# Performance work log

Measured on AMD Instinct MI355X. Metric: run time of the kernel, lower is better.

## Reference

```python
import jax, jax.numpy as jnp
import numpy as np

HIDDEN = 7168
N_HEADS = 32
QK_NOPE = 128
QK_ROPE = 64
V_DIM = 128
Q_LORA = 1536
KV_LORA = 512
ROPE_THETA = 10000.0
EPS = 1e-6
T = 2048
W_SCALE = 0.02


def setup_inputs() -> dict:
    key = jax.random.key(0)
    ks = jax.random.split(key, 8)
    return {
        "hidden_states": jax.random.normal(ks[0], (T, HIDDEN), jnp.float32),
        "positions": jnp.arange(T, dtype=jnp.int32),
        "wq_a": jax.random.normal(ks[1], (HIDDEN, Q_LORA), jnp.float32) * W_SCALE,
        "q_a_ln_w": jnp.ones((Q_LORA,), jnp.float32),
        "wq_b": jax.random.normal(ks[2], (Q_LORA, N_HEADS * (QK_NOPE + QK_ROPE)), jnp.float32) * W_SCALE,
        "wkv_a": jax.random.normal(ks[3], (HIDDEN, KV_LORA + QK_ROPE), jnp.float32) * W_SCALE,
        "kv_a_ln_w": jnp.ones((KV_LORA,), jnp.float32),
        "wkv_b": jax.random.normal(ks[4], (KV_LORA, N_HEADS * (QK_NOPE + V_DIM)), jnp.float32) * W_SCALE,
        "wo": jax.random.normal(ks[5], (N_HEADS * V_DIM, HIDDEN), jnp.float32) * W_SCALE,
    }


def _rmsnorm(x, w, eps=EPS):
    var = jnp.mean(jnp.square(x), axis=-1, keepdims=True)
    return x * jax.lax.rsqrt(var + eps) * w


def _rope_cos_sin(positions):
    # deepseek rope: base**(arange(0, d, 2)/d), interleaved (non-neox) layout
    inv_freq = 1.0 / (ROPE_THETA ** (jnp.arange(0, QK_ROPE, 2, dtype=jnp.float32) / QK_ROPE))
    ang = positions.astype(jnp.float32)[:, None] * inv_freq[None, :]  # [T, 32]
    return jnp.cos(ang), jnp.sin(ang)


def _apply_rope_interleaved(x, cos, sin):
    # x: [T, H, QK_ROPE]; even/odd interleaved pairs
    x1 = x[..., 0::2]
    x2 = x[..., 1::2]
    c = cos[:, None, :]
    s = sin[:, None, :]
    o1 = x1 * c - x2 * s
    o2 = x1 * s + x2 * c
    return jnp.stack([o1, o2], axis=-1).reshape(x.shape)


def reference(hidden_states, positions, wq_a, q_a_ln_w, wq_b, wkv_a, kv_a_ln_w, wkv_b, wo):
    scaling = (QK_NOPE + QK_ROPE) ** -0.5
    # q low-rank path: a-proj -> RMSNorm -> b-proj
    q = _rmsnorm(hidden_states @ wq_a, q_a_ln_w) @ wq_b  # [T, H*192]
    q = q.reshape(T, N_HEADS, QK_NOPE + QK_ROPE)
    q_nope, q_rope = q[..., :QK_NOPE], q[..., QK_NOPE:]
    # kv low-rank path
    latent = hidden_states @ wkv_a  # [T, KV_LORA + QK_ROPE]
    c_kv, k_rope = latent[:, :KV_LORA], latent[:, KV_LORA:]
    c_kv = _rmsnorm(c_kv, kv_a_ln_w)
    # decoupled RoPE on q_rope and shared k_rope
    cos, sin = _rope_cos_sin(positions)
    q_rope = _apply_rope_interleaved(q_rope, cos, sin)
    k_rope = _apply_rope_interleaved(k_rope[:, None, :], cos, sin)  # [T,1,64]
    # expand latent to per-head k_nope and v (kv_b_proj)
    kv = (c_kv @ wkv_b).reshape(T, N_HEADS, QK_NOPE + V_DIM)
    k_nope, v = kv[..., :QK_NOPE], kv[..., QK_NOPE:]
    k = jnp.concatenate([k_nope, jnp.broadcast_to(k_rope, (T, N_HEADS, QK_ROPE))], axis=-1)
    qf = jnp.concatenate([q_nope, q_rope], axis=-1)  # [T,H,192]
    # causal MHA
    scores = jnp.einsum("qhd,khd->hqk", qf, k) * scaling
    mask = jnp.tril(jnp.ones((T, T), dtype=bool))
    scores = jnp.where(mask[None], scores, -jnp.inf)
    p = jax.nn.softmax(scores, axis=-1)
    attn = jnp.einsum("hqk,khd->qhd", p, v).reshape(T, N_HEADS * V_DIM)
    return attn @ wo  # [T, HIDDEN]
```

## Files before the change

kernel.cpp:

```cpp
#include <hip/hip_runtime.h>
#include <stdint.h>

#define T_SEQ 2048
#define HID 7168
#define NH 32
#define DN 128
#define DR 64
#define DQK 192
#define DV 128
#define QL 1536
#define KVL 512
#define LATD 576
#define QD 6144
#define KVD 8192
#define WOK 4096
#define NCAT 2112

typedef unsigned short u16;
typedef __bf16 bf16x8 __attribute__((ext_vector_type(8)));
typedef float f32x4 __attribute__((ext_vector_type(4)));

__device__ __forceinline__ u16 f2bf(float f) {
  union { float f; unsigned u; } v; v.f = f;
  unsigned r = v.u + 0x7FFFu + ((v.u >> 16) & 1u);
  return (u16)(r >> 16);
}
__device__ __forceinline__ float bf2f(u16 s) {
  union { unsigned u; float f; } v; v.u = ((unsigned)s) << 16;
  return v.f;
}

__device__ __forceinline__ void gl2lds16(const void* g, void* l) {
  __builtin_amdgcn_global_load_lds((const __attribute__((address_space(1))) void*)g,
                                   (__attribute__((address_space(3))) void*)l, 16, 0, 0);
}

__device__ __forceinline__ f32x4 mfma16(bf16x8 a, bf16x8 b, f32x4 c) {
  return __builtin_amdgcn_mfma_f32_16x16x32_bf16(a, b, c, 0, 0, 0);
}

__device__ __forceinline__ void store_out(float* p, float v) { *p = v; }
__device__ __forceinline__ void store_out(u16* p, float v) { *p = f2bf(v); }

#define FENCE() asm volatile("" ::: "memory")

__global__ __launch_bounds__(256) void k_cvt_bf16(const float* __restrict__ in,
                                                  u16* __restrict__ out, long long n) {
  long long i = ((long long)blockIdx.x * 256 + threadIdx.x) * 8;
  if (i >= n) return;
  const float4* p = (const float4*)(in + i);
  float4 a = p[0], b = p[1];
  union { uint4 v; u16 s[8]; } o;
  o.s[0]=f2bf(a.x); o.s[1]=f2bf(a.y); o.s[2]=f2bf(a.z); o.s[3]=f2bf(a.w);
  o.s[4]=f2bf(b.x); o.s[5]=f2bf(b.y); o.s[6]=f2bf(b.z); o.s[7]=f2bf(b.w);
  *(uint4*)(out + i) = o.v;
}

__global__ __launch_bounds__(256) void k_transpose_bf16(const float* __restrict__ in,
                                                        u16* __restrict__ out, int R, int C,
                                                        float scale) {
  __shared__ float tile[64][65];
  int c0 = blockIdx.x * 64, r0 = blockIdx.y * 64;
  int tx = threadIdx.x & 15, ty = threadIdx.x >> 4;
  #pragma unroll
  for (int i = 0; i < 4; i++) {
    int r = ty + i * 16;
    float4 v = *(const float4*)(in + (size_t)(r0 + r) * C + c0 + tx * 4);
    tile[r][tx*4+0] = v.x; tile[r][tx*4+1] = v.y; tile[r][tx*4+2] = v.z; tile[r][tx*4+3] = v.w;
  }
  __syncthreads();
  #pragma unroll
  for (int i = 0; i < 4; i++) {
    int oc = ty + i * 16;
    union { uint2 v; u16 s[4]; } o;
    #pragma unroll
    for (int j = 0; j < 4; j++) o.s[j] = f2bf(tile[tx*4+j][oc] * scale);
    *(uint2*)(out + (size_t)(c0 + oc) * R + r0 + tx * 4) = o.v;
  }
}

__global__ __launch_bounds__(256) void k_rmsnorm_bf16(const float* __restrict__ x,
                                                      const float* __restrict__ w,
                                                      u16* __restrict__ out, int n, int ldin) {
  int row = blockIdx.x;
  const float* xr = x + (size_t)row * ldin;
  u16* orow = out + (size_t)row * n;
  float ss = 0.f;
  for (int i = threadIdx.x * 4; i < n; i += 1024) {
    float4 v = *(const float4*)(xr + i);
    ss += v.x*v.x + v.y*v.y + v.z*v.z + v.w*v.w;
  }
  #pragma unroll
  for (int off = 32; off > 0; off >>= 1) ss += __shfl_xor(ss, off);
  __shared__ float red[4];
  if ((threadIdx.x & 63) == 0) red[threadIdx.x >> 6] = ss;
  __syncthreads();
  float tot = red[0] + red[1] + red[2] + red[3];
  float rstd = rsqrtf(tot / (float)n + 1e-6f);
  for (int i = threadIdx.x * 4; i < n; i += 1024) {
    float4 v = *(const float4*)(xr + i);
    float4 g = *(const float4*)(w + i);
    union { uint2 u; u16 s[4]; } o;
    o.s[0]=f2bf(v.x*rstd*g.x); o.s[1]=f2bf(v.y*rstd*g.y);
    o.s[2]=f2bf(v.z*rstd*g.z); o.s[3]=f2bf(v.w*rstd*g.w);
    *(uint2*)(orow + i) = o.u;
  }
}

__global__ __launch_bounds__(256) void k_gemm_bt(const u16* __restrict__ A,
                                                 const u16* __restrict__ Bt,
                                                 float* __restrict__ C,
                                                 int M, int N, int K) {
  __shared__ __attribute__((aligned(16))) u16 As[128 * 32];
  __shared__ __attribute__((aligned(16))) u16 Bs[128 * 32];
  int m0 = blockIdx.y * 128, n0 = blockIdx.x * 128;
  int tid = threadIdx.x;
  int w = tid >> 6, lane = tid & 63, l16 = lane & 15, lh = lane >> 4;
  int wr = (w >> 1) * 64, wc = (w & 1) * 64;
  f32x4 zero = {0.f, 0.f, 0.f, 0.f};
  f32x4 acc[4][4];
  #pragma unroll
  for (int i = 0; i < 4; i++)
    #pragma unroll
    for (int j = 0; j < 4; j++) acc[i][j] = zero;
  int ra = tid >> 2, ca = (tid & 3) * 8;
  const u16* a0 = A + (size_t)(m0 + ra) * K + ca;
  const u16* a1 = A + (size_t)(m0 + ra + 64) * K + ca;
  int rb0 = n0 + ra;      rb0 = rb0 < N ? rb0 : N - 1;
  int rb1 = n0 + ra + 64; rb1 = rb1 < N ? rb1 : N - 1;
  const u16* b0 = Bt + (size_t)rb0 * K + ca;
  const u16* b1 = Bt + (size_t)rb1 * K + ca;
  for (int k0 = 0; k0 < K; k0 += 32) {
    gl2lds16(a0 + k0, &As[tid * 8]);
    gl2lds16(a1 + k0, &As[2048 + tid * 8]);
    gl2lds16(b0 + k0, &Bs[tid * 8]);
    gl2lds16(b1 + k0, &Bs[2048 + tid * 8]);
    __syncthreads();
    bf16x8 af[4], bv[4];
    #pragma unroll
    for (int i = 0; i < 4; i++) af[i] = *(const bf16x8*)&As[(wr + i * 16 + l16) * 32 + lh * 8];
    #pragma unroll
    for (int j = 0; j < 4; j++) bv[j] = *(const bf16x8*)&Bs[(wc + j * 16 + l16) * 32 + lh * 8];
    #pragma unroll
    for (int i = 0; i < 4; i++)
      #pragma unroll
      for (int j = 0; j < 4; j++)
        acc[i][j] = mfma16(af[i], bv[j], acc[i][j]);
    __syncthreads();
  }
  #pragma unroll
  for (int i = 0; i < 4; i++) {
    #pragma unroll
    for (int j = 0; j < 4; j++) {
      int col = n0 + wc + j * 16 + l16;
      if (col < N) {
        #pragma unroll
        for (int r = 0; r < 4; r++) {
          int row = m0 + wr + i * 16 + lh * 4 + r;
          C[(size_t)row * N + col] = acc[i][j][r];
        }
      }
    }
  }
}

template <typename OutT>
__global__ __launch_bounds__(512) void k_gemm_bt256(const u16* __restrict__ A,
                                                    const u16* __restrict__ Bt,
                                                    OutT* __restrict__ C,
                                                    int N, int K) {
  __shared__ __attribute__((aligned(16))) u16 lds[3 * 16384];
  const int tid = threadIdx.x;
  const int lane = tid & 63, l16 = lane & 15, lh = lane >> 4;
  const int w = tid >> 6, wm = w >> 2, wn = w & 3;
  const int m0 = blockIdx.y * 256, n0 = blockIdx.x * 256;
  const int nt = K >> 5;

  f32x4 acc[8][4];
  #pragma unroll
  for (int i = 0; i < 8; i++)
    #pragma unroll
    for (int j = 0; j < 4; j++) acc[i][j] = f32x4{0.f, 0.f, 0.f, 0.f};

  const int P = tid * 16;
  const int ls = P ^ (((P >> 7) & 7) << 4);
  const int sr = ls >> 6;
  const int sce = (ls & 63) >> 1;
  const u16* gA0 = A + (size_t)(m0 + sr) * K + sce;
  const u16* gA1 = A + (size_t)(m0 + sr + 128) * K + sce;
  const u16* gB0 = Bt + (size_t)(n0 + sr) * K + sce;
  const u16* gB1 = Bt + (size_t)(n0 + sr + 128) * K + sce;
  u16* ldst = &lds[tid * 8];

  for (int pt = 0; pt < 2 && pt < nt; ++pt) {
    gl2lds16(gA0 + pt * 32, ldst + pt * 16384);
    gl2lds16(gA1 + pt * 32, ldst + pt * 16384 + 4096);
    gl2lds16(gB0 + pt * 32, ldst + pt * 16384 + 8192);
    gl2lds16(gB1 + pt * 32, ldst + pt * 16384 + 12288);
  }
  __syncthreads();

  int bufr = 0;
  for (int t = 0; t < nt; ++t) {
    const bool more = (t + 2) < nt;
    const int bw = (t + 2) % 3;
    const u16* As = &lds[bufr * 16384];
    const u16* Bs = &lds[bufr * 16384 + 8192];
    bf16x8 afr[4], bfr[4];
    #pragma unroll
    for (int j = 0; j < 4; ++j) {
      int L = ((wn * 64 + j * 16 + l16) << 6) + (lh << 4);
      bfr[j] = *(const bf16x8*)((const char*)Bs + (L ^ (((L >> 7) & 7) << 4)));
    }
    #pragma unroll
    for (int i = 0; i < 4; ++i) {
      int L = ((wm * 128 + i * 16 + l16) << 6) + (lh << 4);
      afr[i] = *(const bf16x8*)((const char*)As + (L ^ (((L >> 7) & 7) << 4)));
    }
    if (more) {
      gl2lds16(gA0 + (t + 2) * 32, ldst + bw * 16384);
      gl2lds16(gA1 + (t + 2) * 32, ldst + bw * 16384 + 4096);
    }
    FENCE();
    __builtin_amdgcn_s_barrier();
    FENCE();
    __builtin_amdgcn_s_setprio(1);
    #pragma unroll
    for (int i = 0; i < 4; ++i)
      #pragma unroll
      for (int j = 0; j < 4; ++j)
        acc[i][j] = mfma16(afr[i], bfr[j], acc[i][j]);
    __builtin_amdgcn_s_setprio(0);
    FENCE();
    __builtin_amdgcn_s_barrier();
    FENCE();
    #pragma unroll
    for (int i = 0; i < 4; ++i) {
      int L = ((wm * 128 + 64 + i * 16 + l16) << 6) + (lh << 4);
      afr[i] = *(const bf16x8*)((const char*)As + (L ^ (((L >> 7) & 7) << 4)));
    }
    if (more) {
      gl2lds16(gB0 + (t + 2) * 32, ldst + bw * 16384 + 8192);
      gl2lds16(gB1 + (t + 2) * 32, ldst + bw * 16384 + 12288);
    }
    FENCE();
    __builtin_amdgcn_s_barrier();
    FENCE();
    __builtin_amdgcn_s_setprio(1);
    #pragma unroll
    for (int i = 0; i < 4; ++i)
      #pragma unroll
      for (int j = 0; j < 4; ++j)
        acc[4 + i][j] = mfma16(afr[i], bfr[j], acc[4 + i][j]);
    __builtin_amdgcn_s_setprio(0);
    FENCE();
    if (more) asm volatile("s_waitcnt vmcnt(4)" ::: "memory");
    else      asm volatile("s_waitcnt vmcnt(0)" ::: "memory");
    __builtin_amdgcn_s_barrier();
    FENCE();
    bufr = (bufr == 2) ? 0 : bufr + 1;
  }

  #pragma unroll
  for (int hf = 0; hf < 2; ++hf) {
    #pragma unroll
    for (int i = 0; i < 4; ++i) {
      int rbase = m0 + wm * 128 + hf * 64 + i * 16 + lh * 4;
      #pragma unroll
      for (int j = 0; j < 4; ++j) {
        int col = n0 + wn * 64 + j * 16 + l16;
        #pragma unroll
        for (int r = 0; r < 4; ++r)
          store_out(&C[(size_t)(rbase + r) * N + col], acc[hf * 4 + i][j][r]);
      }
    }
  }
}

__global__ __launch_bounds__(256) void k_build_q(const u16* __restrict__ qf,
                                                 const int* __restrict__ pos,
                                                 u16* __restrict__ Qc) {
  int t = blockIdx.x;
  __shared__ float cs[32], sn[32];
  if (threadIdx.x < 32) {
    float inv = expf(-9.2103403719761836f * (float)threadIdx.x / 32.f);
    float ang = (float)pos[t] * inv;
    cs[threadIdx.x] = cosf(ang);
    sn[threadIdx.x] = sinf(ang);
  }
  __syncthreads();
  const u16* qrow = qf + (size_t)t * QD;
  for (int e = threadIdx.x; e < QD; e += 256) {
    int h = e / 192, d = e - h * 192;
    u16 outv;
    if (d < DN) {
      outv = qrow[e];
    } else {
      int dr = d - DN, i = dr >> 1;
      float x1 = bf2f(qrow[h * 192 + DN + 2 * i]), x2 = bf2f(qrow[h * 192 + DN + 2 * i + 1]);
      float v = (dr & 1) ? (x1 * sn[i] + x2 * cs[i]) : (x1 * cs[i] - x2 * sn[i]);
      outv = f2bf(v);
    }
    Qc[((size_t)h * T_SEQ + t) * DQK + d] = outv;
  }
}

__global__ __launch_bounds__(256) void k_build_k(const u16* __restrict__ kvf,
                                                 const float* __restrict__ kr, int krld,
                                                 const int* __restrict__ pos,
                                                 u16* __restrict__ Kc) {
  int t = blockIdx.x;
  __shared__ u16 kro[64];
  if (threadIdx.x < 32) {
    int i = threadIdx.x;
    float inv = expf(-9.2103403719761836f * (float)i / 32.f);
    float ang = (float)pos[t] * inv;
    float c = cosf(ang), s = sinf(ang);
    float x1 = kr[(size_t)t * krld + 2 * i];
    float x2 = kr[(size_t)t * krld + 2 * i + 1];
    kro[2 * i]     = f2bf(x1 * c - x2 * s);
    kro[2 * i + 1] = f2bf(x1 * s + x2 * c);
  }
  __syncthreads();
  const u16* krow = kvf + (size_t)t * KVD;
  for (int e = threadIdx.x; e < NH * DQK; e += 256) {
    int h = e / 192, d = e - h * 192;
    Kc[((size_t)h * T_SEQ + t) * DQK + d] = (d < DN) ? krow[h * 256 + d] : kro[d - DN];
  }
}

__global__ __launch_bounds__(256) void k_build_vt(const u16* __restrict__ kvf,
                                                  u16* __restrict__ Vt) {
  __shared__ unsigned tile[64][65];
  int t0 = blockIdx.x * 64, d0 = blockIdx.y * 64, h = blockIdx.z;
  int tid = threadIdx.x;
  #pragma unroll
  for (int i = 0; i < 2; i++) {
    int r = (tid >> 3) + i * 32;
    int c = (tid & 7) * 8;
    uint4 v = *(const uint4*)(kvf + (size_t)(t0 + r) * KVD + h * 256 + DN + d0 + c);
    const u16* s = (const u16*)&v;
    #pragma unroll
    for (int j = 0; j < 8; j++) tile[r][c + j] = s[j];
  }
  __syncthreads();
  #pragma unroll
  for (int i = 0; i < 2; i++) {
    int d = (tid >> 3) + i * 32;
    int tb = (tid & 7) * 8;
    union { uint4 v; u16 s[8]; } o;
    #pragma unroll
    for (int j = 0; j < 8; j++) o.s[j] = (u16)tile[tb + j][d];
    *(uint4*)(Vt + ((size_t)h * DV + d0 + d) * T_SEQ + t0 + tb) = o.v;
  }
}

__global__ __launch_bounds__(256, 2) void k_mla_attn(const u16* __restrict__ Qc,
                                                     const u16* __restrict__ Kc,
                                                     const u16* __restrict__ Vt,
                                                     u16* __restrict__ attn) {
  __shared__ __attribute__((aligned(16))) u16 Ks[2 * 64 * 192];
  __shared__ __attribute__((aligned(16))) u16 Ps[64 * 64];
  int bid = blockIdx.x;
  int hi = bid >> 8, r = bid & 255;
  int qt = 31 - (r >> 3);
  int h = (hi << 3) | (r & 7);
  int tid = threadIdx.x, w = tid >> 6, lane = tid & 63, l16 = lane & 15, lh = lane >> 4;
  int swz = (l16 & 7) << 4;

  const char* Kb = (const char*)(Kc + (size_t)h * T_SEQ * DQK);
  const u16* Vh = Vt + (size_t)h * DV * T_SEQ;

  const char* Qg = (const char*)(Qc + ((size_t)h * T_SEQ + (size_t)qt * 64) * DQK);
  #pragma unroll
  for (int i = 0; i < 6; i++) {
    int L = tid * 16 + i * 4096;
    int row = L / 384;
    gl2lds16(Qg + (L ^ ((row & 7) << 4)), (char*)Ks + L);
  }
  #pragma unroll
  for (int i = 0; i < 6; i++) {
    int L = tid * 16 + i * 4096;
    int row = L / 384;
    gl2lds16(Kb + (L ^ ((row & 7) << 4)), (char*)Ks + 24576 + L);
  }
  __syncthreads();
  bf16x8 aq[6];
  #pragma unroll
  for (int kf = 0; kf < 6; kf++)
    aq[kf] = *(const bf16x8*)((const char*)Ks + (w * 16 + l16) * 384 + ((kf * 64 + lh * 16) ^ swz));
  __syncthreads();

  f32x4 zero = {0.f, 0.f, 0.f, 0.f};
  f32x4 accO[8];
  #pragma unroll
  for (int i = 0; i < 8; i++) accO[i] = zero;
  float m[4]    = {-3e38f, -3e38f, -3e38f, -3e38f};
  float lsum[4] = {0.f, 0.f, 0.f, 0.f};

  for (int kt = 0; kt <= qt; ++kt) {
    const char* Kcur = (const char*)Ks + (1 - (kt & 1)) * 24576;
    char* Kstg = (char*)Ks + (kt & 1) * 24576;
    if (kt < qt) {
      const char* Kg = Kb + (size_t)(kt + 1) * 64 * DQK * 2;
      #pragma unroll
      for (int i = 0; i < 6; i++) {
        int L = tid * 16 + i * 4096;
        int row = L / 384;
        gl2lds16(Kg + (L ^ ((row & 7) << 4)), Kstg + L);
      }
    }
    bf16x8 vf[16];
    #pragma unroll
    for (int of = 0; of < 8; ++of)
      #pragma unroll
      for (int kf = 0; kf < 2; ++kf)
        vf[of * 2 + kf] = *(const bf16x8*)(Vh + (size_t)(of * 16 + l16) * T_SEQ +
                                           kt * 64 + kf * 32 + lh * 8);

    f32x4 sf[4];
    #pragma unroll
    for (int j = 0; j < 4; j++) sf[j] = zero;
    #pragma unroll
    for (int kf = 0; kf < 6; ++kf) {
      #pragma unroll
      for (int j = 0; j < 4; ++j) {
        bf16x8 bk = *(const bf16x8*)(Kcur + (j * 16 + l16) * 384 + ((kf * 64 + lh * 16) ^ swz));
        sf[j] = mfma16(aq[kf], bk, sf[j]);
      }
    }
    bool diag = (kt == qt);
    #pragma unroll
    for (int rr = 0; rr < 4; ++rr) {
      int qrow = qt * 64 + w * 16 + lh * 4 + rr;
      float rowm = -3e38f;
      #pragma unroll
      for (int j = 0; j < 4; ++j) {
        float s = sf[j][rr];
        if (diag && (kt * 64 + j * 16 + l16) > qrow) s = -3e38f;
        sf[j][rr] = s;
        rowm = fmaxf(rowm, s);
      }
      rowm = fmaxf(rowm, __shfl_xor(rowm, 1));
      rowm = fmaxf(rowm, __shfl_xor(rowm, 2));
      rowm = fmaxf(rowm, __shfl_xor(rowm, 4));
      rowm = fmaxf(rowm, __shfl_xor(rowm, 8));
      float mnew = fmaxf(m[rr], rowm);
      float sc = __expf(m[rr] - mnew);
      float pj[4];
      float ps = 0.f;
      #pragma unroll
      for (int j = 0; j < 4; ++j) { pj[j] = __expf(sf[j][rr] - mnew); ps += pj[j]; }
      ps += __shfl_xor(ps, 1); ps += __shfl_xor(ps, 2);
      ps += __shfl_xor(ps, 4); ps += __shfl_xor(ps, 8);
      lsum[rr] = lsum[rr] * sc + ps;
      m[rr] = mnew;
      #pragma unroll
      for (int of = 0; of < 8; ++of) accO[of][rr] *= sc;
      int rw = w * 16 + lh * 4 + rr;
      int rsw = (rw & 7) << 4;
      #pragma unroll
      for (int j = 0; j < 4; ++j)
        *(u16*)((char*)Ps + rw * 128 + ((2 * (j * 16 + l16)) ^ rsw)) = f2bf(pj[j]);
    }
    #pragma unroll
    for (int kf = 0; kf < 2; ++kf) {
      bf16x8 ap = *(const bf16x8*)((const char*)Ps + (w * 16 + l16) * 128 +
                                   ((kf * 64 + lh * 16) ^ swz));
      #pragma unroll
      for (int of = 0; of < 8; ++of)
        accO[of] = mfma16(ap, vf[of * 2 + kf], accO[of]);
    }
    __syncthreads();
  }
  #pragma unroll
  for (int rr = 0; rr < 4; ++rr) {
    float inv = 1.f / lsum[rr];
    int t = qt * 64 + w * 16 + lh * 4 + rr;
    #pragma unroll
    for (int of = 0; of < 8; ++of)
      attn[(size_t)t * WOK + h * DV + of * 16 + l16] = f2bf(accO[of][rr] * inv);
  }
}

extern "C" void kernel_launch(void* const* d_in, const int* in_sizes, int n_in,
                              void* d_out, int out_size, void* d_ws, size_t ws_size,
                              hipStream_t stream) {
  const float* hidden     = (const float*)d_in[0];
  const int*   positions  = (const int*)d_in[1];
  const float* wq_a       = (const float*)d_in[2];
  const float* q_a_ln_w   = (const float*)d_in[3];
  const float* wq_b       = (const float*)d_in[4];
  const float* wkv_a      = (const float*)d_in[5];
  const float* kv_a_ln_w  = (const float*)d_in[6];
  const float* wkv_b      = (const float*)d_in[7];
  const float* wo         = (const float*)d_in[8];
  float* out = (float*)d_out;

  char* p = (char*)d_ws;
  size_t off = 0;
  auto alloc = [&](size_t bytes) -> void* {
    void* r = p + off;
    off += (bytes + 255) & ~(size_t)255;
    return r;
  };
  u16*   h_bf = (u16*)  alloc((size_t)T_SEQ * HID * 2);
  u16*   wbuf = (u16*)  alloc((size_t)HID * WOK * 2);
  u16*   bigh = (u16*)  alloc((size_t)T_SEQ * KVD * 2);
  float* cat  = (float*)alloc((size_t)T_SEQ * NCAT * 4);
  u16*   qln  = (u16*)  alloc((size_t)T_SEQ * QL * 2);
  u16*   ckv  = (u16*)  alloc((size_t)T_SEQ * KVL * 2);
  u16*   Qc   = (u16*)  alloc((size_t)NH * T_SEQ * DQK * 2);
  u16*   Kc   = (u16*)  alloc((size_t)NH * T_SEQ * DQK * 2);
  u16*   Vt   = (u16*)  alloc((size_t)NH * DV * T_SEQ * 2);
  u16*   attn = (u16*)  alloc((size_t)T_SEQ * WOK * 2);

  k_cvt_bf16<<<(T_SEQ * HID) / (256 * 8), 256, 0, stream>>>(hidden, h_bf, (long long)T_SEQ * HID);

  k_transpose_bf16<<<dim3(QL / 64, HID / 64), 256, 0, stream>>>(wq_a, wbuf, HID, QL, 1.0f);
  k_transpose_bf16<<<dim3(LATD / 64, HID / 64), 256, 0, stream>>>(wkv_a, wbuf + (size_t)QL * HID,
                                                                  HID, LATD, 1.0f);
  k_gemm_bt<<<dim3((NCAT + 127) / 128, T_SEQ / 128), 256, 0, stream>>>(h_bf, wbuf, cat,
                                                                       T_SEQ, NCAT, HID);

  k_rmsnorm_bf16<<<T_SEQ, 256, 0, stream>>>(cat + QL, kv_a_ln_w, ckv, KVL, NCAT);
  k_transpose_bf16<<<dim3(KVD / 64, KVL / 64), 256, 0, stream>>>(wkv_b, wbuf, KVL, KVD, 1.0f);
  k_gemm_bt256<u16><<<dim3(KVD / 256, T_SEQ / 256), 512, 0, stream>>>(ckv, wbuf, bigh, KVD, KVL);
  k_build_k<<<T_SEQ, 256, 0, stream>>>(bigh, cat + QL + KVL, NCAT, positions, Kc);
  k_build_vt<<<dim3(T_SEQ / 64, 2, NH), 256, 0, stream>>>(bigh, Vt);

  k_rmsnorm_bf16<<<T_SEQ, 256, 0, stream>>>(cat, q_a_ln_w, qln, QL, NCAT);
  k_transpose_bf16<<<dim3(QD / 64, QL / 64), 256, 0, stream>>>(wq_b, wbuf, QL, QD,
                                                               0.07216878364870322f);
  k_gemm_bt256<u16><<<dim3(QD / 256, T_SEQ / 256), 512, 0, stream>>>(qln, wbuf, bigh, QD, QL);
  k_build_q<<<T_SEQ, 256, 0, stream>>>(bigh, positions, Qc);

  k_mla_attn<<<1024, 256, 0, stream>>>(Qc, Kc, Vt, attn);

  k_transpose_bf16<<<dim3(HID / 64, WOK / 64), 256, 0, stream>>>(wo, wbuf, WOK, HID, 1.0f);
  k_gemm_bt256<float><<<dim3(HID / 256, T_SEQ / 256), 512, 0, stream>>>(attn, wbuf, out, HID, WOK);
}
```

Before: 684.1 us.

## Transpose QK^T MFMA so each lane owns one query row; lazy softmax rescale

Swaps the MFMA operands in the score computation so each lane holds a full query row's scores. This lets the row max and sum reductions use two cross-lane shuffles instead of per-row four-step shuffles. It skips the output rescale unless the running max grows by more than a threshold, writes P to LDS as packed 8-byte stores, and adds s_setprio around the MFMA sections. The lazy rescale relies on the exponentials staying bounded by exp(8), and the per-row scale now needs shuffles to reach the accumulator layout.

```diff
diff --git a/kernel.cpp b/kernel.cpp
--- a/kernel.cpp
+++ b/kernel.cpp
@@ -395,8 +395,10 @@
   f32x4 accO[8];
   #pragma unroll
   for (int i = 0; i < 8; i++) accO[i] = zero;
-  float m[4]    = {-3e38f, -3e38f, -3e38f, -3e38f};
-  float lsum[4] = {0.f, 0.f, 0.f, 0.f};
+  float m_q = -3e38f;
+  float lsum = 0.f;
+
+  const int qg = qt * 64 + w * 16 + l16;
 
   for (int kt = 0; kt <= qt; ++kt) {
     const char* Kcur = (const char*)Ks + (1 - (kt & 1)) * 24576;
@@ -421,48 +423,57 @@
     f32x4 sf[4];
     #pragma unroll
     for (int j = 0; j < 4; j++) sf[j] = zero;
+    __builtin_amdgcn_s_setprio(1);
     #pragma unroll
     for (int kf = 0; kf < 6; ++kf) {
       #pragma unroll
       for (int j = 0; j < 4; ++j) {
         bf16x8 bk = *(const bf16x8*)(Kcur + (j * 16 + l16) * 384 + ((kf * 64 + lh * 16) ^ swz));
-        sf[j] = mfma16(aq[kf], bk, sf[j]);
+        sf[j] = mfma16(bk, aq[kf], sf[j]);
       }
     }
+    __builtin_amdgcn_s_setprio(0);
+
     bool diag = (kt == qt);
-    #pragma unroll
-    for (int rr = 0; rr < 4; ++rr) {
-      int qrow = qt * 64 + w * 16 + lh * 4 + rr;
-      float rowm = -3e38f;
-      #pragma unroll
-      for (int j = 0; j < 4; ++j) {
+    float p[16];
+    float rowm = -3e38f;
+    #pragma unroll
+    for (int j = 0; j < 4; ++j)
+      #pragma unroll
+      for (int rr = 0; rr < 4; ++rr) {
         float s = sf[j][rr];
-        if (diag && (kt * 64 + j * 16 + l16) > qrow) s = -3e38f;
-        sf[j][rr] = s;
+        if (diag && (kt * 64 + j * 16 + lh * 4 + rr) > qg) s = -3e38f;
+        p[j * 4 + rr] = s;
         rowm = fmaxf(rowm, s);
       }
-      rowm = fmaxf(rowm, __shfl_xor(rowm, 1));
-      rowm = fmaxf(rowm, __shfl_xor(rowm, 2));
-      rowm = fmaxf(rowm, __shfl_xor(rowm, 4));
-      rowm = fmaxf(rowm, __shfl_xor(rowm, 8));
-      float mnew = fmaxf(m[rr], rowm);
-      float sc = __expf(m[rr] - mnew);
-      float pj[4];
-      float ps = 0.f;
-      #pragma unroll
-      for (int j = 0; j < 4; ++j) { pj[j] = __expf(sf[j][rr] - mnew); ps += pj[j]; }
-      ps += __shfl_xor(ps, 1); ps += __shfl_xor(ps, 2);
-      ps += __shfl_xor(ps, 4); ps += __shfl_xor(ps, 8);
-      lsum[rr] = lsum[rr] * sc + ps;
-      m[rr] = mnew;
-      #pragma unroll
-      for (int of = 0; of < 8; ++of) accO[of][rr] *= sc;
-      int rw = w * 16 + lh * 4 + rr;
-      int rsw = (rw & 7) << 4;
-      #pragma unroll
-      for (int j = 0; j < 4; ++j)
-        *(u16*)((char*)Ps + rw * 128 + ((2 * (j * 16 + l16)) ^ rsw)) = f2bf(pj[j]);
-    }
+    rowm = fmaxf(rowm, __shfl_xor(rowm, 16));
+    rowm = fmaxf(rowm, __shfl_xor(rowm, 32));
+    if (!__all(rowm <= m_q + 8.f)) {
+      float mnew = fmaxf(m_q, rowm);
+      float sc = __expf(m_q - mnew);
+      m_q = mnew;
+      lsum *= sc;
+      #pragma unroll
+      for (int rr = 0; rr < 4; ++rr) {
+        float scr = __shfl(sc, (lane & 48) | (lh * 4 + rr));
+        #pragma unroll
+        for (int of = 0; of < 8; ++of) accO[of][rr] *= scr;
+      }
+    }
+    float ps = 0.f;
+    #pragma unroll
+    for (int i = 0; i < 16; ++i) { p[i] = __expf(p[i] - m_q); ps += p[i]; }
+    ps += __shfl_xor(ps, 16);
+    ps += __shfl_xor(ps, 32);
+    lsum += ps;
+    #pragma unroll
+    for (int j = 0; j < 4; ++j) {
+      union { uint2 u; u16 s[4]; } pw;
+      #pragma unroll
+      for (int rr = 0; rr < 4; ++rr) pw.s[rr] = f2bf(p[j * 4 + rr]);
+      *(uint2*)((char*)Ps + (w * 16 + l16) * 128 + ((j * 32 + lh * 8) ^ swz)) = pw.u;
+    }
+    __builtin_amdgcn_s_setprio(1);
     #pragma unroll
     for (int kf = 0; kf < 2; ++kf) {
       bf16x8 ap = *(const bf16x8*)((const char*)Ps + (w * 16 + l16) * 128 +
@@ -471,15 +482,17 @@
       for (int of = 0; of < 8; ++of)
         accO[of] = mfma16(ap, vf[of * 2 + kf], accO[of]);
     }
+    __builtin_amdgcn_s_setprio(0);
     __syncthreads();
   }
+  float inv = 1.f / lsum;
   #pragma unroll
   for (int rr = 0; rr < 4; ++rr) {
-    float inv = 1.f / lsum[rr];
+    float invr = __shfl(inv, (lane & 48) | (lh * 4 + rr));
     int t = qt * 64 + w * 16 + lh * 4 + rr;
     #pragma unroll
     for (int of = 0; of < 8; ++of)
-      attn[(size_t)t * WOK + h * DV + of * 16 + l16] = f2bf(accO[of][rr] * inv);
+      attn[(size_t)t * WOK + h * DV + of * 16 + l16] = f2bf(accO[of][rr] * invr);
   }
 }
 
```

New measurement: 704.2 us. +2.9%, slower.

## Use 128-row query tiles with 8 waves sharing K tiles in attention

Applied to the files above, without the earlier changes.

The attention kernel now gives each block 128 query rows across 8 waves, so every K tile loaded into LDS serves twice as many queries. Q is read straight from global memory into registers instead of being staged through LDS. The causal mask is now checked on every tile, and s_setprio is raised around the MFMA sections. The trade-off is more LDS for P, wasted work on the extra half-masked tile per block, per-element mask checks on all tiles, and fewer blocks for load balancing.

```diff
diff --git a/kernel.cpp b/kernel.cpp
--- a/kernel.cpp
+++ b/kernel.cpp
@@ -355,40 +355,33 @@
   }
 }
 
-__global__ __launch_bounds__(256, 2) void k_mla_attn(const u16* __restrict__ Qc,
+__global__ __launch_bounds__(512, 4) void k_mla_attn(const u16* __restrict__ Qc,
                                                      const u16* __restrict__ Kc,
                                                      const u16* __restrict__ Vt,
                                                      u16* __restrict__ attn) {
   __shared__ __attribute__((aligned(16))) u16 Ks[2 * 64 * 192];
-  __shared__ __attribute__((aligned(16))) u16 Ps[64 * 64];
+  __shared__ __attribute__((aligned(16))) u16 Ps[128 * 64];
   int bid = blockIdx.x;
-  int hi = bid >> 8, r = bid & 255;
-  int qt = 31 - (r >> 3);
-  int h = (hi << 3) | (r & 7);
+  int hi = bid >> 7, low = bid & 127;
+  int qtile = 15 - (low >> 3);
+  int h = (hi << 3) | (low & 7);
   int tid = threadIdx.x, w = tid >> 6, lane = tid & 63, l16 = lane & 15, lh = lane >> 4;
   int swz = (l16 & 7) << 4;
+  int qbase = qtile * 128 + w * 16;
 
   const char* Kb = (const char*)(Kc + (size_t)h * T_SEQ * DQK);
   const u16* Vh = Vt + (size_t)h * DV * T_SEQ;
 
-  const char* Qg = (const char*)(Qc + ((size_t)h * T_SEQ + (size_t)qt * 64) * DQK);
-  #pragma unroll
-  for (int i = 0; i < 6; i++) {
-    int L = tid * 16 + i * 4096;
-    int row = L / 384;
-    gl2lds16(Qg + (L ^ ((row & 7) << 4)), (char*)Ks + L);
-  }
-  #pragma unroll
-  for (int i = 0; i < 6; i++) {
-    int L = tid * 16 + i * 4096;
+  #pragma unroll
+  for (int i = 0; i < 3; i++) {
+    int L = tid * 16 + i * 8192;
     int row = L / 384;
     gl2lds16(Kb + (L ^ ((row & 7) << 4)), (char*)Ks + 24576 + L);
   }
-  __syncthreads();
+  const u16* Qrow = Qc + ((size_t)h * T_SEQ + qbase + l16) * DQK;
   bf16x8 aq[6];
   #pragma unroll
-  for (int kf = 0; kf < 6; kf++)
-    aq[kf] = *(const bf16x8*)((const char*)Ks + (w * 16 + l16) * 384 + ((kf * 64 + lh * 16) ^ swz));
+  for (int kf = 0; kf < 6; kf++) aq[kf] = *(const bf16x8*)(Qrow + kf * 32 + lh * 8);
   __syncthreads();
 
   f32x4 zero = {0.f, 0.f, 0.f, 0.f};
@@ -398,14 +391,15 @@
   float m[4]    = {-3e38f, -3e38f, -3e38f, -3e38f};
   float lsum[4] = {0.f, 0.f, 0.f, 0.f};
 
-  for (int kt = 0; kt <= qt; ++kt) {
+  const int ktmax = 2 * qtile + 1;
+  for (int kt = 0; kt <= ktmax; ++kt) {
     const char* Kcur = (const char*)Ks + (1 - (kt & 1)) * 24576;
     char* Kstg = (char*)Ks + (kt & 1) * 24576;
-    if (kt < qt) {
-      const char* Kg = Kb + (size_t)(kt + 1) * 64 * DQK * 2;
-      #pragma unroll
-      for (int i = 0; i < 6; i++) {
-        int L = tid * 16 + i * 4096;
+    if (kt < ktmax) {
+      const char* Kg = Kb + (size_t)(kt + 1) * (64 * DQK * 2);
+      #pragma unroll
+      for (int i = 0; i < 3; i++) {
+        int L = tid * 16 + i * 8192;
         int row = L / 384;
         gl2lds16(Kg + (L ^ ((row & 7) << 4)), Kstg + L);
       }
@@ -421,6 +415,7 @@
     f32x4 sf[4];
     #pragma unroll
     for (int j = 0; j < 4; j++) sf[j] = zero;
+    __builtin_amdgcn_s_setprio(1);
     #pragma unroll
     for (int kf = 0; kf < 6; ++kf) {
       #pragma unroll
@@ -429,15 +424,16 @@
         sf[j] = mfma16(aq[kf], bk, sf[j]);
       }
     }
-    bool diag = (kt == qt);
+    __builtin_amdgcn_s_setprio(0);
+
     #pragma unroll
     for (int rr = 0; rr < 4; ++rr) {
-      int qrow = qt * 64 + w * 16 + lh * 4 + rr;
+      int qrow = qbase + lh * 4 + rr;
       float rowm = -3e38f;
       #pragma unroll
       for (int j = 0; j < 4; ++j) {
         float s = sf[j][rr];
-        if (diag && (kt * 64 + j * 16 + l16) > qrow) s = -3e38f;
+        if ((kt * 64 + j * 16 + l16) > qrow) s = -3e38f;
         sf[j][rr] = s;
         rowm = fmaxf(rowm, s);
       }
@@ -463,6 +459,7 @@
       for (int j = 0; j < 4; ++j)
         *(u16*)((char*)Ps + rw * 128 + ((2 * (j * 16 + l16)) ^ rsw)) = f2bf(pj[j]);
     }
+    __builtin_amdgcn_s_setprio(1);
     #pragma unroll
     for (int kf = 0; kf < 2; ++kf) {
       bf16x8 ap = *(const bf16x8*)((const char*)Ps + (w * 16 + l16) * 128 +
@@ -471,12 +468,13 @@
       for (int of = 0; of < 8; ++of)
         accO[of] = mfma16(ap, vf[of * 2 + kf], accO[of]);
     }
+    __builtin_amdgcn_s_setprio(0);
     __syncthreads();
   }
   #pragma unroll
   for (int rr = 0; rr < 4; ++rr) {
     float inv = 1.f / lsum[rr];
-    int t = qt * 64 + w * 16 + lh * 4 + rr;
+    int t = qbase + lh * 4 + rr;
     #pragma unroll
     for (int of = 0; of < 8; ++of)
       attn[(size_t)t * WOK + h * DV + of * 16 + l16] = f2bf(accO[of][rr] * inv);
@@ -535,7 +533,7 @@
   k_gemm_bt256<u16><<<dim3(QD / 256, T_SEQ / 256), 512, 0, stream>>>(qln, wbuf, bigh, QD, QL);
   k_build_q<<<T_SEQ, 256, 0, stream>>>(bigh, positions, Qc);
 
-  k_mla_attn<<<1024, 256, 0, stream>>>(Qc, Kc, Vt, attn);
+  k_mla_attn<<<512, 512, 0, stream>>>(Qc, Kc, Vt, attn);
 
   k_transpose_bf16<<<dim3(HID / 64, WOK / 64), 256, 0, stream>>>(wo, wbuf, WOK, HID, 1.0f);
   k_gemm_bt256<float><<<dim3(HID / 256, T_SEQ / 256), 512, 0, stream>>>(attn, wbuf, out, HID, WOK);
```

Result: slower. 1.142 ms (+66.9%).

## Load attention K and Q fragments directly from global memory, drop LDS staging

Applied to the files above, without the earlier changes.

The attention kernel no longer stages Q and K tiles in a double-buffered, swizzled LDS buffer through async global-to-LDS copies. Each wave now reads its Q fragments and the K fragments for every key tile straight from global memory. This removes the per-tile block barrier and the launch-bounds occupancy hint, since only the per-wave P scratch remains in shared memory. The aim is to cut LDS use and synchronisation so more blocks can run concurrently. The cost is that all four waves fetch the same K tile separately, raising L2 traffic, and the explicit prefetch of the next K tile is lost.

```diff
diff --git a/kernel.cpp b/kernel.cpp
--- a/kernel.cpp
+++ b/kernel.cpp
@@ -355,11 +355,10 @@
   }
 }
 
-__global__ __launch_bounds__(256, 2) void k_mla_attn(const u16* __restrict__ Qc,
-                                                     const u16* __restrict__ Kc,
-                                                     const u16* __restrict__ Vt,
-                                                     u16* __restrict__ attn) {
-  __shared__ __attribute__((aligned(16))) u16 Ks[2 * 64 * 192];
+__global__ __launch_bounds__(256) void k_mla_attn(const u16* __restrict__ Qc,
+                                                  const u16* __restrict__ Kc,
+                                                  const u16* __restrict__ Vt,
+                                                  u16* __restrict__ attn) {
   __shared__ __attribute__((aligned(16))) u16 Ps[64 * 64];
   int bid = blockIdx.x;
   int hi = bid >> 8, r = bid & 255;
@@ -368,28 +367,13 @@
   int tid = threadIdx.x, w = tid >> 6, lane = tid & 63, l16 = lane & 15, lh = lane >> 4;
   int swz = (l16 & 7) << 4;
 
-  const char* Kb = (const char*)(Kc + (size_t)h * T_SEQ * DQK);
+  const u16* Kh = Kc + (size_t)h * T_SEQ * DQK;
   const u16* Vh = Vt + (size_t)h * DV * T_SEQ;
 
-  const char* Qg = (const char*)(Qc + ((size_t)h * T_SEQ + (size_t)qt * 64) * DQK);
-  #pragma unroll
-  for (int i = 0; i < 6; i++) {
-    int L = tid * 16 + i * 4096;
-    int row = L / 384;
-    gl2lds16(Qg + (L ^ ((row & 7) << 4)), (char*)Ks + L);
-  }
-  #pragma unroll
-  for (int i = 0; i < 6; i++) {
-    int L = tid * 16 + i * 4096;
-    int row = L / 384;
-    gl2lds16(Kb + (L ^ ((row & 7) << 4)), (char*)Ks + 24576 + L);
-  }
-  __syncthreads();
+  const u16* Qrow = Qc + ((size_t)h * T_SEQ + (size_t)qt * 64 + w * 16 + l16) * DQK;
   bf16x8 aq[6];
   #pragma unroll
-  for (int kf = 0; kf < 6; kf++)
-    aq[kf] = *(const bf16x8*)((const char*)Ks + (w * 16 + l16) * 384 + ((kf * 64 + lh * 16) ^ swz));
-  __syncthreads();
+  for (int kf = 0; kf < 6; kf++) aq[kf] = *(const bf16x8*)(Qrow + kf * 32 + lh * 8);
 
   f32x4 zero = {0.f, 0.f, 0.f, 0.f};
   f32x4 accO[8];
@@ -399,17 +383,6 @@
   float lsum[4] = {0.f, 0.f, 0.f, 0.f};
 
   for (int kt = 0; kt <= qt; ++kt) {
-    const char* Kcur = (const char*)Ks + (1 - (kt & 1)) * 24576;
-    char* Kstg = (char*)Ks + (kt & 1) * 24576;
-    if (kt < qt) {
-      const char* Kg = Kb + (size_t)(kt + 1) * 64 * DQK * 2;
-      #pragma unroll
-      for (int i = 0; i < 6; i++) {
-        int L = tid * 16 + i * 4096;
-        int row = L / 384;
-        gl2lds16(Kg + (L ^ ((row & 7) << 4)), Kstg + L);
-      }
-    }
     bf16x8 vf[16];
     #pragma unroll
     for (int of = 0; of < 8; ++of)
@@ -425,7 +398,8 @@
     for (int kf = 0; kf < 6; ++kf) {
       #pragma unroll
       for (int j = 0; j < 4; ++j) {
-        bf16x8 bk = *(const bf16x8*)(Kcur + (j * 16 + l16) * 384 + ((kf * 64 + lh * 16) ^ swz));
+        bf16x8 bk = *(const bf16x8*)(Kh + (size_t)(kt * 64 + j * 16 + l16) * DQK +
+                                     kf * 32 + lh * 8);
         sf[j] = mfma16(aq[kf], bk, sf[j]);
       }
     }
@@ -471,7 +445,6 @@
       for (int of = 0; of < 8; ++of)
         accO[of] = mfma16(ap, vf[of * 2 + kf], accO[of]);
     }
-    __syncthreads();
   }
   #pragma unroll
   for (int rr = 0; rr < 4; ++rr) {
```

Result: slower. 951.8 us (+39.1%).
